# Kernel tuning notes

Measured on AMD Instinct MI355X. Metric: run time of the kernel, lower is better.

## Reference

```python
import jax, jax.numpy as jnp
import numpy as np

N_NODES = 50000


def _sage_conv(x, src, dst, W_l, b_l, W_r, n_nodes):
    # mean-aggregate neighbor (source) features onto targets
    msg = x[src]                                   # [E, d_in] gather
    agg = jax.ops.segment_sum(msg, dst, num_segments=n_nodes)   # [N, d_in]
    deg = jax.ops.segment_sum(jnp.ones((src.shape[0],), x.dtype), dst,
                              num_segments=n_nodes)
    agg = agg / jnp.clip(deg, 1.0, None)[:, None]  # mean with deg>=1 clamp (PyG)
    # out = lin_l(agg) + lin_r(x)   (bias lives in lin_l)
    return agg @ W_l.T + b_l + x @ W_r.T


def setup_inputs() -> dict:
    key = jax.random.key(0)
    ks = jax.random.split(key, 8)
    d_in, d_hid, d_out = 128, 256, 128
    n_edges = 800000
    x = jax.random.normal(ks[0], (N_NODES, d_in), dtype=jnp.float32)
    edge_index = jax.random.randint(ks[1], (2, n_edges), 0, N_NODES, dtype=jnp.int32)
    def glorot(k, shape):
        lim = float(np.sqrt(6.0 / (shape[0] + shape[1])))
        return jax.random.uniform(k, shape, jnp.float32, -lim, lim)
    return {
        "x": x,
        "edge_index": edge_index,
        "W1l": glorot(ks[2], (d_hid, d_in)),
        "b1": jnp.zeros((d_hid,), jnp.float32),
        "W1r": glorot(ks[3], (d_hid, d_in)),
        "W2l": glorot(ks[4], (d_out, d_hid)),
        "b2": jnp.zeros((d_out,), jnp.float32),
        "W2r": glorot(ks[5], (d_out, d_hid)),
    }


def reference(x, edge_index, W1l, b1, W1r, W2l, b2, W2r):
    src, dst = edge_index[0], edge_index[1]
    h = jax.nn.relu(_sage_conv(x, src, dst, W1l, b1, W1r, N_NODES))
    out = _sage_conv(h, src, dst, W2l, b2, W2r, N_NODES)
    return out
```

## Files before the change

kernel.cpp:

```cpp
#include <hip/hip_runtime.h>
#include <hip/hip_bf16.h>

#define NN 50000
#define NN_PAD 50176
#define NE 800000
#define NB 196
#define NB2 784
#define CAP2 1536
#define ECAP 2048
#define EPB 4096

typedef __attribute__((ext_vector_type(8))) short short8;
typedef __attribute__((ext_vector_type(8))) unsigned short ushort8;
typedef __attribute__((ext_vector_type(4))) float f32x4;
typedef __attribute__((ext_vector_type(2))) float f32x2;
typedef __attribute__((ext_vector_type(4))) unsigned int u32x4;
typedef __attribute__((ext_vector_type(2))) unsigned int u32x2;

__device__ __forceinline__ unsigned short f2bf(float f) {
    union { float f; unsigned u; } v; v.f = f;
    unsigned u = v.u;
    return (unsigned short)((u + 0x7fffu + ((u >> 16) & 1u)) >> 16);
}
__device__ __forceinline__ float bfu_lo(unsigned u) {
    union { unsigned u; float f; } v; v.u = u << 16; return v.f;
}
__device__ __forceinline__ float bfu_hi(unsigned u) {
    union { unsigned u; float f; } v; v.u = u & 0xffff0000u; return v.f;
}
__device__ __forceinline__ void acc_fp8(float* acc, uint2 q) {
    f32x2 a0 = __builtin_amdgcn_cvt_pk_f32_fp8(q.x, false);
    f32x2 a1 = __builtin_amdgcn_cvt_pk_f32_fp8(q.x, true);
    f32x2 a2 = __builtin_amdgcn_cvt_pk_f32_fp8(q.y, false);
    f32x2 a3 = __builtin_amdgcn_cvt_pk_f32_fp8(q.y, true);
    acc[0] += a0.x; acc[1] += a0.y; acc[2] += a1.x; acc[3] += a1.y;
    acc[4] += a2.x; acc[5] += a2.y; acc[6] += a3.x; acc[7] += a3.y;
}



__global__ void k_setup_part(const float* __restrict__ W1l, const float* __restrict__ W1r,
                             const float* __restrict__ W2l, const float* __restrict__ W2r,
                             unsigned short* __restrict__ W1pk, unsigned short* __restrict__ W2pk,
                             const float* __restrict__ x, unsigned short* __restrict__ Apk,
                             unsigned char* __restrict__ x_f8,
                             const int* __restrict__ src, const int* __restrict__ dst,
                             int* __restrict__ gcursor, unsigned* __restrict__ pairs) {
    int blk = blockIdx.x, t = threadIdx.x;
    if (blk < NB) {
        __shared__ int cnt[NB2];
        __shared__ int cur[NB2];
        __shared__ int base[NB2];
        for (int k = t; k < NB2; k += 256) { cnt[k] = 0; cur[k] = 0; }
        __syncthreads();
        int e0 = blk * EPB;
        int eend = min(e0 + EPB, NE);
        for (int e = e0 + t; e < eend; e += 256)
            atomicAdd(&cnt[dst[e] >> 6], 1);
        __syncthreads();
        for (int k = t; k < NB2; k += 256)
            if (cnt[k] > 0) base[k] = k * CAP2 + atomicAdd(&gcursor[k], cnt[k]);
        __syncthreads();
        for (int e = e0 + t; e < eend; e += 256) {
            int s = src[e], d = dst[e];
            int bk = d >> 6;
            int pos = base[bk] + atomicAdd(&cur[bk], 1);
            if (pos < (bk + 1) * CAP2) pairs[pos] = ((unsigned)s << 6) | (unsigned)(d & 63);
        }
    } else if (blk < 260) {
        int tid = (blk - 196) * 256 + t;
        int table = tid >> 13;
        int r = tid & 8191;
        int lane = r & 63, ni = (r >> 6) & 3, ks = (r >> 8) & 7, g = r >> 11;
        int lm = lane & 15, lq = lane >> 4;
        int o = g * 64 + ni * 16 + lm;
        int k = ks * 32 + lq * 8;
        unsigned short v[8];
        if (table == 0) {
            if (k < 128) {
#pragma unroll
                for (int j = 0; j < 8; ++j) v[j] = f2bf(W1l[o * 128 + k + j]);
            } else {
#pragma unroll
                for (int j = 0; j < 8; ++j) v[j] = f2bf(W1r[o * 128 + k - 128 + j]);
            }
            *(uint4*)(W1pk + (size_t)r * 8) = *(const uint4*)v;
        } else {
            if (o < 128) {
#pragma unroll
                for (int j = 0; j < 8; ++j) v[j] = f2bf(W2l[o * 256 + k + j]);
            } else {
#pragma unroll
                for (int j = 0; j < 8; ++j) v[j] = f2bf(W2r[(o - 128) * 256 + k + j]);
            }
            *(uint4*)(W2pk + (size_t)r * 8) = *(const uint4*)v;
        }
    } else {
        int gid = (blk - 260) * 256 + t;
        int nq = gid >> 7, r128 = gid & 127;
        int n = nq * 4 + (r128 & 3), c = r128 >> 2;
        f32x4 v = __builtin_nontemporal_load((const f32x4*)x + (size_t)n * 32 + c);
        unsigned short o[4];
        o[0] = f2bf(v[0]); o[1] = f2bf(v[1]); o[2] = f2bf(v[2]); o[3] = f2bf(v[3]);
        int k = 128 + c * 4;
        int ks = k >> 5, lq = (k >> 3) & 3, j0 = k & 7;
        int tile = n >> 6, r = n & 63, mi = r >> 4, lm = r & 15;
        *(u32x2*)(Apk + (size_t)tile * 16384 +
                  ((size_t)((ks * 4 + mi) * 64 + lm + 16 * lq)) * 8 + j0) = *(const u32x2*)o;
        unsigned p = (unsigned)__builtin_amdgcn_cvt_pk_fp8_f32(v[0], v[1], 0, false);
        p = (unsigned)__builtin_amdgcn_cvt_pk_fp8_f32(v[2], v[3], (int)p, true);
        *(unsigned*)(x_f8 + (size_t)n * 128 + c * 4) = p;
    }
}

__global__ __launch_bounds__(512) void k_build_agg1(
        const int* __restrict__ gcursor, const unsigned* __restrict__ pairs,
        const uint2* __restrict__ xf8, unsigned short* __restrict__ esrc,
        unsigned* __restrict__ meta, unsigned short* __restrict__ Apk) {
    __shared__ unsigned lp[CAP2];
    __shared__ __align__(16) unsigned short lsrc[ECAP];
    __shared__ int ldeg[64];
    __shared__ int lcur[64];
    __shared__ int lstart[64];
    int b = blockIdx.x, t = threadIdx.x;
    if (t < 64) ldeg[t] = 0;
    __syncthreads();
    int cnt = min(gcursor[b], CAP2);
    const unsigned* pb = pairs + (size_t)b * CAP2;
    for (int e = t; e < cnt; e += 512) {
        unsigned p = pb[e];
        lp[e] = p;
        atomicAdd(&ldeg[p & 63u], 1);
    }
    __syncthreads();
    if (t < 64) {
        int s = 0;
        for (int j = 0; j < t; ++j) s += (ldeg[j] + 7) & ~7;
        lstart[t] = s; lcur[t] = s;
    }
    __syncthreads();
    for (int e = t; e < cnt; e += 512) {
        unsigned p = lp[e];
        int pos = atomicAdd(&lcur[p & 63u], 1);
        lsrc[pos] = (unsigned short)(p >> 6);
    }
    __syncthreads();
    int lim = lstart[63] + ldeg[63];
    for (int e = t; e < lim; e += 512) esrc[(size_t)b * ECAP + e] = lsrc[e];
    if (t < 64) {
        int node = b * 64 + t;
        if (node < NN)
            meta[node] = ((unsigned)(b * ECAP + lstart[t])) | ((unsigned)ldeg[t] << 21);
    }
    int c = t & 15, h = (t >> 4) & 1;
#pragma unroll
    for (int rr = 0; rr < 4; ++rr) {
        int nl = rr * 16 + (t >> 5);
        int st = lstart[nl], dg = ldeg[nl];
        float acc[8] = {0.f, 0.f, 0.f, 0.f, 0.f, 0.f, 0.f, 0.f};
        int nbt = dg >> 3;
        for (int k = h; k < nbt; k += 2) {
            ushort8 sv = *(const ushort8*)(lsrc + st + k * 8);
            uint2 q0 = xf8[(size_t)sv[0] * 16 + c];
            uint2 q1 = xf8[(size_t)sv[1] * 16 + c];
            uint2 q2 = xf8[(size_t)sv[2] * 16 + c];
            uint2 q3 = xf8[(size_t)sv[3] * 16 + c];
            uint2 q4 = xf8[(size_t)sv[4] * 16 + c];
            uint2 q5 = xf8[(size_t)sv[5] * 16 + c];
            uint2 q6 = xf8[(size_t)sv[6] * 16 + c];
            uint2 q7 = xf8[(size_t)sv[7] * 16 + c];
            acc_fp8(acc, q0); acc_fp8(acc, q1); acc_fp8(acc, q2); acc_fp8(acc, q3);
            acc_fp8(acc, q4); acc_fp8(acc, q5); acc_fp8(acc, q6); acc_fp8(acc, q7);
        }
        if (h == (nbt & 1)) {
            for (int i = nbt * 8; i < dg; ++i)
                acc_fp8(acc, xf8[(size_t)lsrc[st + i] * 16 + c]);
        }
#pragma unroll
        for (int j = 0; j < 8; ++j) acc[j] += __shfl_xor(acc[j], 16);
        if (h == 0) {
            float invd = 1.0f / (float)max(dg, 1);
            unsigned short o[8];
#pragma unroll
            for (int j = 0; j < 8; ++j) o[j] = f2bf(acc[j] * invd);
            int ks = c >> 2, lq = c & 3;
            int mi = nl >> 4, lm = nl & 15;
            *(u32x4*)(Apk + (size_t)b * 16384 +
                      ((size_t)((ks * 4 + mi) * 64 + lm + 16 * lq)) * 8) = *(const u32x4*)o;
        }
    }
}

__global__ __launch_bounds__(256, 2) void k_gemm12(
        const unsigned short* __restrict__ Apk,
        const unsigned short* __restrict__ W1pk, const unsigned short* __restrict__ W2pk,
        const float* __restrict__ b1, const float* __restrict__ b2,
        unsigned char* __restrict__ y2f8, unsigned short* __restrict__ Sbf) {
    __shared__ unsigned short T[16384];
    int t = threadIdx.x, blk = blockIdx.x;
    int wave = t >> 6, lane = t & 63;
    int lm = lane & 15, lq = lane >> 4;
    int pbase = lm * 4 + lq;

    short8 w[8][4];
    {
        const unsigned short* wb = W1pk + (size_t)wave * 16384;
#pragma unroll
        for (int ks = 0; ks < 8; ++ks)
#pragma unroll
            for (int ni = 0; ni < 4; ++ni)
                w[ks][ni] = *(const short8*)(wb + ((size_t)((ks * 4 + ni) * 64 + lane)) * 8);
    }

    const unsigned short* apk = Apk + (size_t)blk * 16384;
    f32x4 acc1[4][4];
#pragma unroll
    for (int mi = 0; mi < 4; ++mi)
#pragma unroll
        for (int ni = 0; ni < 4; ++ni) acc1[mi][ni] = (f32x4){0.f, 0.f, 0.f, 0.f};
#pragma unroll
    for (int ks = 0; ks < 8; ++ks) {
        short8 a[4];
#pragma unroll
        for (int mi = 0; mi < 4; ++mi)
            a[mi] = *(const short8*)(apk + ((size_t)((ks * 4 + mi) * 64 + lane)) * 8);
#pragma unroll
        for (int mi = 0; mi < 4; ++mi)
#pragma unroll
            for (int ni = 0; ni < 4; ++ni)
                acc1[mi][ni] = __builtin_amdgcn_mfma_f32_16x16x32_bf16(a[mi], w[ks][ni], acc1[mi][ni], 0, 0, 0);
    }

    {
        const unsigned short* wb = W2pk + (size_t)wave * 16384;
#pragma unroll
        for (int ks = 0; ks < 8; ++ks)
#pragma unroll
            for (int ni = 0; ni < 4; ++ni)
                w[ks][ni] = *(const short8*)(wb + ((size_t)((ks * 4 + ni) * 64 + lane)) * 8);
    }

#pragma unroll
    for (int ni = 0; ni < 4; ++ni) {
        int col = wave * 64 + ni * 16 + lm;
        float bv = b1[col];
        int ks = col >> 5;
        int la = (col & 31) >> 3, j = col & 7;
#pragma unroll
        for (int mi = 0; mi < 4; ++mi)
#pragma unroll
            for (int r = 0; r < 4; ++r) {
                float v = fmaxf(acc1[mi][ni][r] + bv, 0.0f);
                T[((size_t)((ks * 4 + mi) * 64 + (lq * 4 + r) * 4 + la)) * 8 + j] = f2bf(v);
            }
    }
    __syncthreads();

    f32x4 acc2[4][4];
#pragma unroll
    for (int mi = 0; mi < 4; ++mi)
#pragma unroll
        for (int ni = 0; ni < 4; ++ni) acc2[mi][ni] = (f32x4){0.f, 0.f, 0.f, 0.f};
#pragma unroll
    for (int ks = 0; ks < 8; ++ks) {
        short8 a[4];
#pragma unroll
        for (int mi = 0; mi < 4; ++mi)
            a[mi] = *(const short8*)(T + ((size_t)((ks * 4 + mi) * 64 + pbase)) * 8);
#pragma unroll
        for (int mi = 0; mi < 4; ++mi)
#pragma unroll
            for (int ni = 0; ni < 4; ++ni)
                acc2[mi][ni] = __builtin_amdgcn_mfma_f32_16x16x32_bf16(a[mi], w[ks][ni], acc2[mi][ni], 0, 0, 0);
    }
    __syncthreads();

    {
        unsigned char* T8 = (unsigned char*)T;
        unsigned short* T16 = (unsigned short*)T + 4096;
        if (wave < 2) {
#pragma unroll
            for (int ni = 0; ni < 4; ++ni) {
                int col = wave * 64 + ni * 16 + lm;
#pragma unroll
                for (int mi = 0; mi < 4; ++mi)
#pragma unroll
                    for (int r = 0; r < 4; ++r) {
                        int rl = mi * 16 + lq * 4 + r;
                        float v = acc2[mi][ni][r];
                        unsigned p = (unsigned)__builtin_amdgcn_cvt_pk_fp8_f32(v, v, 0, false);
                        T8[rl * 128 + col] = (unsigned char)(p & 0xff);
                    }
            }
        } else {
#pragma unroll
            for (int ni = 0; ni < 4; ++ni) {
                int col = (wave - 2) * 64 + ni * 16 + lm;
                float bv = b2[col];
#pragma unroll
                for (int mi = 0; mi < 4; ++mi)
#pragma unroll
                    for (int r = 0; r < 4; ++r) {
                        int rl = mi * 16 + lq * 4 + r;
                        T16[rl * 128 + col] = f2bf(acc2[mi][ni][r] + bv);
                    }
            }
        }
    }
    __syncthreads();

    {
        const uint4* Ty = (const uint4*)T;
        uint4* gy = (uint4*)(y2f8 + (size_t)blk * 64 * 128);
        gy[t] = Ty[t];
        gy[t + 256] = Ty[t + 256];
        const u32x4* Ts = (const u32x4*)((const char*)T + 8192);
        u32x4* gs = (u32x4*)(Sbf + (size_t)blk * 64 * 128);
#pragma unroll
        for (int i = 0; i < 4; ++i)
            __builtin_nontemporal_store(Ts[t + i * 256], &gs[t + i * 256]);
    }
}

__global__ void k_agg_out(const uint2* __restrict__ yf8, const unsigned short* __restrict__ Sbf,
                          const unsigned* __restrict__ meta,
                          const unsigned short* __restrict__ esrc,
                          float* __restrict__ out) {
    int gid = blockIdx.x * blockDim.x + threadIdx.x;
    int n = gid >> 5, sub = gid & 31, c = sub & 15, h = sub >> 4;
    unsigned mt = meta[n];
    int st = (int)(mt & 0x1FFFFFu), dg = (int)(mt >> 21);
    float acc[8] = {0.f, 0.f, 0.f, 0.f, 0.f, 0.f, 0.f, 0.f};
    int nbt = dg >> 3;
    for (int k = h; k < nbt; k += 2) {
        ushort8 sv = *(const ushort8*)(esrc + (size_t)st + (size_t)k * 8);
        uint2 q0 = yf8[(size_t)sv[0] * 16 + c];
        uint2 q1 = yf8[(size_t)sv[1] * 16 + c];
        uint2 q2 = yf8[(size_t)sv[2] * 16 + c];
        uint2 q3 = yf8[(size_t)sv[3] * 16 + c];
        uint2 q4 = yf8[(size_t)sv[4] * 16 + c];
        uint2 q5 = yf8[(size_t)sv[5] * 16 + c];
        uint2 q6 = yf8[(size_t)sv[6] * 16 + c];
        uint2 q7 = yf8[(size_t)sv[7] * 16 + c];
        acc_fp8(acc, q0); acc_fp8(acc, q1); acc_fp8(acc, q2); acc_fp8(acc, q3);
        acc_fp8(acc, q4); acc_fp8(acc, q5); acc_fp8(acc, q6); acc_fp8(acc, q7);
    }
    if (h == (nbt & 1)) {
        for (int i = nbt * 8; i < dg; ++i)
            acc_fp8(acc, yf8[(size_t)esrc[st + i] * 16 + c]);
    }
#pragma unroll
    for (int j = 0; j < 8; ++j) acc[j] += __shfl_xor(acc[j], 16);
    float invd = 1.0f / (float)max(dg, 1);
    float s0 = h ? acc[4] : acc[0];
    float s1 = h ? acc[5] : acc[1];
    float s2 = h ? acc[6] : acc[2];
    float s3 = h ? acc[7] : acc[3];
    int colb = c * 8 + h * 4;
    u32x2 sv2 = *(const u32x2*)(Sbf + (size_t)n * 128 + colb);
    f32x4 o;
    o[0] = bfu_lo(sv2[0]) + s0 * invd; o[1] = bfu_hi(sv2[0]) + s1 * invd;
    o[2] = bfu_lo(sv2[1]) + s2 * invd; o[3] = bfu_hi(sv2[1]) + s3 * invd;
    __builtin_nontemporal_store(o, (f32x4*)(out + (size_t)n * 128 + colb));
}

extern "C" void kernel_launch(void* const* d_in, const int* in_sizes, int n_in,
                              void* d_out, int out_size, void* d_ws, size_t ws_size,
                              hipStream_t stream) {
    const float* x   = (const float*)d_in[0];
    const int*   ei  = (const int*)d_in[1];
    const int*   src = ei;
    const int*   dst = ei + NE;
    const float* W1l = (const float*)d_in[2];
    const float* b1  = (const float*)d_in[3];
    const float* W1r = (const float*)d_in[4];
    const float* W2l = (const float*)d_in[5];
    const float* b2  = (const float*)d_in[6];
    const float* W2r = (const float*)d_in[7];
    float* out = (float*)d_out;

    char* ws = (char*)d_ws;
    int* gcursor          = (int*)(ws + 0);
    unsigned* meta        = (unsigned*)(ws + 4096);
    unsigned* pairs       = (unsigned*)(ws + 204800);
    unsigned short* esrc  = (unsigned short*)(ws + 5021696);
    unsigned char* x_f8   = (unsigned char*)(ws + 8232960);
    unsigned short* Sbf   = (unsigned short*)(ws + 14632960);
    unsigned char* y2f8   = (unsigned char*)(ws + 27478016);
    unsigned short* Apk   = (unsigned short*)(ws + 33900544);
    unsigned short* W1pk  = (unsigned short*)(ws + 59590656);
    unsigned short* W2pk  = (unsigned short*)(ws + 59721728);

    hipMemsetAsync(gcursor, 0, 4096, stream);
    k_setup_part<<<6510, 256, 0, stream>>>(W1l, W1r, W2l, W2r, W1pk, W2pk,
                                           x, Apk, x_f8, src, dst, gcursor, pairs);
    k_build_agg1<<<NB2, 512, 0, stream>>>(gcursor, pairs, (const uint2*)x_f8,
                                          esrc, meta, Apk);
    k_gemm12<<<NB2, 256, 0, stream>>>(Apk, W1pk, W2pk, b1, b2, y2f8, Sbf);
    k_agg_out<<<NN * 32 / 256, 256, 0, stream>>>((const uint2*)y2f8, Sbf,
                                                 meta, esrc, out);
}
```

Baseline: 197.1 us.

## Fuse CSR build and layer-1 aggregation into GEMM kernel via LDS A-tile

Merges the per-bucket CSR build and layer-1 mean aggregation into the fused GEMM kernel. The aggregated bf16 rows now go straight into an LDS tile alongside a separately packed self-feature tile, so the aggregated half of the A matrix no longer round-trips through global memory and one launch disappears. Both gather loops drop the two-thread split per feature chunk in favour of one thread per 8-column chunk, which removes the shuffle reduction. The cost is fewer threads covering each node's gather, so each thread walks longer serial loops, and the fused kernel uses 256 threads where the build kernel had 512.

```diff
diff --git a/kernel.cpp b/kernel.cpp
--- a/kernel.cpp
+++ b/kernel.cpp
@@ -42,7 +42,7 @@
 __global__ void k_setup_part(const float* __restrict__ W1l, const float* __restrict__ W1r,
                              const float* __restrict__ W2l, const float* __restrict__ W2r,
                              unsigned short* __restrict__ W1pk, unsigned short* __restrict__ W2pk,
-                             const float* __restrict__ x, unsigned short* __restrict__ Apk,
+                             const float* __restrict__ x, unsigned short* __restrict__ Aslf,
                              unsigned char* __restrict__ x_f8,
                              const int* __restrict__ src, const int* __restrict__ dst,
                              int* __restrict__ gcursor, unsigned* __restrict__ pairs) {
@@ -97,41 +97,41 @@
         }
     } else {
         int gid = (blk - 260) * 256 + t;
-        int nq = gid >> 7, r128 = gid & 127;
-        int n = nq * 4 + (r128 & 3), c = r128 >> 2;
+        int n = gid >> 5, c = gid & 31;
         f32x4 v = __builtin_nontemporal_load((const f32x4*)x + (size_t)n * 32 + c);
         unsigned short o[4];
         o[0] = f2bf(v[0]); o[1] = f2bf(v[1]); o[2] = f2bf(v[2]); o[3] = f2bf(v[3]);
-        int k = 128 + c * 4;
-        int ks = k >> 5, lq = (k >> 3) & 3, j0 = k & 7;
         int tile = n >> 6, r = n & 63, mi = r >> 4, lm = r & 15;
-        *(u32x2*)(Apk + (size_t)tile * 16384 +
-                  ((size_t)((ks * 4 + mi) * 64 + lm + 16 * lq)) * 8 + j0) = *(const u32x2*)o;
+        int ck = (c >> 3) * 4 + mi;
+        int lq = (c >> 1) & 3, j0 = 4 * (c & 1);
+        *(u32x2*)(Aslf + (size_t)tile * 8192 +
+                  ((size_t)(ck * 64 + lm + 16 * lq)) * 8 + j0) = *(const u32x2*)o;
         unsigned p = (unsigned)__builtin_amdgcn_cvt_pk_fp8_f32(v[0], v[1], 0, false);
         p = (unsigned)__builtin_amdgcn_cvt_pk_fp8_f32(v[2], v[3], (int)p, true);
         *(unsigned*)(x_f8 + (size_t)n * 128 + c * 4) = p;
     }
 }
 
-__global__ __launch_bounds__(512) void k_build_agg1(
+__global__ __launch_bounds__(256, 2) void k_bagg_gemm(
         const int* __restrict__ gcursor, const unsigned* __restrict__ pairs,
-        const uint2* __restrict__ xf8, unsigned short* __restrict__ esrc,
-        unsigned* __restrict__ meta, unsigned short* __restrict__ Apk) {
-    __shared__ unsigned lp[CAP2];
+        const uint2* __restrict__ xf8, const unsigned short* __restrict__ Aslf,
+        const unsigned short* __restrict__ W1pk, const unsigned short* __restrict__ W2pk,
+        const float* __restrict__ b1, const float* __restrict__ b2,
+        unsigned short* __restrict__ esrc, unsigned* __restrict__ meta,
+        unsigned char* __restrict__ y2f8, unsigned short* __restrict__ Sbf) {
+    __shared__ unsigned short LA[16384];
     __shared__ __align__(16) unsigned short lsrc[ECAP];
     __shared__ int ldeg[64];
     __shared__ int lcur[64];
     __shared__ int lstart[64];
     int b = blockIdx.x, t = threadIdx.x;
+
     if (t < 64) ldeg[t] = 0;
     __syncthreads();
     int cnt = min(gcursor[b], CAP2);
     const unsigned* pb = pairs + (size_t)b * CAP2;
-    for (int e = t; e < cnt; e += 512) {
-        unsigned p = pb[e];
-        lp[e] = p;
-        atomicAdd(&ldeg[p & 63u], 1);
-    }
+    for (int e = t; e < cnt; e += 256)
+        atomicAdd(&ldeg[pb[e] & 63u], 1);
     __syncthreads();
     if (t < 64) {
         int s = 0;
@@ -139,69 +139,62 @@
         lstart[t] = s; lcur[t] = s;
     }
     __syncthreads();
-    for (int e = t; e < cnt; e += 512) {
-        unsigned p = lp[e];
+    for (int e = t; e < cnt; e += 256) {
+        unsigned p = pb[e];
         int pos = atomicAdd(&lcur[p & 63u], 1);
         lsrc[pos] = (unsigned short)(p >> 6);
     }
     __syncthreads();
     int lim = lstart[63] + ldeg[63];
-    for (int e = t; e < lim; e += 512) esrc[(size_t)b * ECAP + e] = lsrc[e];
+    for (int e = t; e < lim; e += 256) esrc[(size_t)b * ECAP + e] = lsrc[e];
     if (t < 64) {
         int node = b * 64 + t;
         if (node < NN)
             meta[node] = ((unsigned)(b * ECAP + lstart[t])) | ((unsigned)ldeg[t] << 21);
     }
-    int c = t & 15, h = (t >> 4) & 1;
-#pragma unroll
-    for (int rr = 0; rr < 4; ++rr) {
-        int nl = rr * 16 + (t >> 5);
-        int st = lstart[nl], dg = ldeg[nl];
-        float acc[8] = {0.f, 0.f, 0.f, 0.f, 0.f, 0.f, 0.f, 0.f};
-        int nbt = dg >> 3;
-        for (int k = h; k < nbt; k += 2) {
-            ushort8 sv = *(const ushort8*)(lsrc + st + k * 8);
-            uint2 q0 = xf8[(size_t)sv[0] * 16 + c];
-            uint2 q1 = xf8[(size_t)sv[1] * 16 + c];
-            uint2 q2 = xf8[(size_t)sv[2] * 16 + c];
-            uint2 q3 = xf8[(size_t)sv[3] * 16 + c];
-            uint2 q4 = xf8[(size_t)sv[4] * 16 + c];
-            uint2 q5 = xf8[(size_t)sv[5] * 16 + c];
-            uint2 q6 = xf8[(size_t)sv[6] * 16 + c];
-            uint2 q7 = xf8[(size_t)sv[7] * 16 + c];
-            acc_fp8(acc, q0); acc_fp8(acc, q1); acc_fp8(acc, q2); acc_fp8(acc, q3);
-            acc_fp8(acc, q4); acc_fp8(acc, q5); acc_fp8(acc, q6); acc_fp8(acc, q7);
-        }
-        if (h == (nbt & 1)) {
-            for (int i = nbt * 8; i < dg; ++i)
+
+    {
+        int c = t & 15;
+#pragma unroll
+        for (int rr = 0; rr < 4; ++rr) {
+            int nl = rr * 16 + (t >> 4);
+            int st = lstart[nl], dg = ldeg[nl];
+            float acc[8] = {0.f, 0.f, 0.f, 0.f, 0.f, 0.f, 0.f, 0.f};
+            int i = 0;
+            for (; i + 8 <= dg; i += 8) {
+                ushort8 sv = *(const ushort8*)(lsrc + st + i);
+                uint2 q0 = xf8[(size_t)sv[0] * 16 + c];
+                uint2 q1 = xf8[(size_t)sv[1] * 16 + c];
+                uint2 q2 = xf8[(size_t)sv[2] * 16 + c];
+                uint2 q3 = xf8[(size_t)sv[3] * 16 + c];
+                uint2 q4 = xf8[(size_t)sv[4] * 16 + c];
+                uint2 q5 = xf8[(size_t)sv[5] * 16 + c];
+                uint2 q6 = xf8[(size_t)sv[6] * 16 + c];
+                uint2 q7 = xf8[(size_t)sv[7] * 16 + c];
+                acc_fp8(acc, q0); acc_fp8(acc, q1); acc_fp8(acc, q2); acc_fp8(acc, q3);
+                acc_fp8(acc, q4); acc_fp8(acc, q5); acc_fp8(acc, q6); acc_fp8(acc, q7);
+            }
+            for (; i < dg; ++i)
                 acc_fp8(acc, xf8[(size_t)lsrc[st + i] * 16 + c]);
-        }
-#pragma unroll
-        for (int j = 0; j < 8; ++j) acc[j] += __shfl_xor(acc[j], 16);
-        if (h == 0) {
             float invd = 1.0f / (float)max(dg, 1);
             unsigned short o[8];
 #pragma unroll
             for (int j = 0; j < 8; ++j) o[j] = f2bf(acc[j] * invd);
-            int ks = c >> 2, lq = c & 3;
-            int mi = nl >> 4, lm = nl & 15;
-            *(u32x4*)(Apk + (size_t)b * 16384 +
-                      ((size_t)((ks * 4 + mi) * 64 + lm + 16 * lq)) * 8) = *(const u32x4*)o;
+            int ks = c >> 2, lq2 = c & 3;
+            int mi = nl >> 4, lm2 = nl & 15;
+            *(u32x4*)(LA + ((size_t)((ks * 4 + mi) * 64 + lm2 + 16 * lq2)) * 8) = *(const u32x4*)o;
         }
     }
-}
-
-__global__ __launch_bounds__(256, 2) void k_gemm12(
-        const unsigned short* __restrict__ Apk,
-        const unsigned short* __restrict__ W1pk, const unsigned short* __restrict__ W2pk,
-        const float* __restrict__ b1, const float* __restrict__ b2,
-        unsigned char* __restrict__ y2f8, unsigned short* __restrict__ Sbf) {
-    __shared__ unsigned short T[16384];
-    int t = threadIdx.x, blk = blockIdx.x;
+    {
+        const u32x4* g = (const u32x4*)(Aslf + (size_t)b * 8192);
+        u32x4* d = (u32x4*)(LA + 8192);
+#pragma unroll
+        for (int i = 0; i < 4; ++i) d[t + i * 256] = g[t + i * 256];
+    }
+
     int wave = t >> 6, lane = t & 63;
     int lm = lane & 15, lq = lane >> 4;
     int pbase = lm * 4 + lq;
-
     short8 w[8][4];
     {
         const unsigned short* wb = W1pk + (size_t)wave * 16384;
@@ -211,8 +204,8 @@
             for (int ni = 0; ni < 4; ++ni)
                 w[ks][ni] = *(const short8*)(wb + ((size_t)((ks * 4 + ni) * 64 + lane)) * 8);
     }
-
-    const unsigned short* apk = Apk + (size_t)blk * 16384;
+    __syncthreads();
+
     f32x4 acc1[4][4];
 #pragma unroll
     for (int mi = 0; mi < 4; ++mi)
@@ -223,7 +216,7 @@
         short8 a[4];
 #pragma unroll
         for (int mi = 0; mi < 4; ++mi)
-            a[mi] = *(const short8*)(apk + ((size_t)((ks * 4 + mi) * 64 + lane)) * 8);
+            a[mi] = *(const short8*)(LA + ((size_t)((ks * 4 + mi) * 64 + lane)) * 8);
 #pragma unroll
         for (int mi = 0; mi < 4; ++mi)
 #pragma unroll
@@ -239,6 +232,7 @@
             for (int ni = 0; ni < 4; ++ni)
                 w[ks][ni] = *(const short8*)(wb + ((size_t)((ks * 4 + ni) * 64 + lane)) * 8);
     }
+    __syncthreads();
 
 #pragma unroll
     for (int ni = 0; ni < 4; ++ni) {
@@ -251,7 +245,7 @@
 #pragma unroll
             for (int r = 0; r < 4; ++r) {
                 float v = fmaxf(acc1[mi][ni][r] + bv, 0.0f);
-                T[((size_t)((ks * 4 + mi) * 64 + (lq * 4 + r) * 4 + la)) * 8 + j] = f2bf(v);
+                LA[((size_t)((ks * 4 + mi) * 64 + (lq * 4 + r) * 4 + la)) * 8 + j] = f2bf(v);
             }
     }
     __syncthreads();
@@ -266,7 +260,7 @@
         short8 a[4];
 #pragma unroll
         for (int mi = 0; mi < 4; ++mi)
-            a[mi] = *(const short8*)(T + ((size_t)((ks * 4 + mi) * 64 + pbase)) * 8);
+            a[mi] = *(const short8*)(LA + ((size_t)((ks * 4 + mi) * 64 + pbase)) * 8);
 #pragma unroll
         for (int mi = 0; mi < 4; ++mi)
 #pragma unroll
@@ -276,8 +270,8 @@
     __syncthreads();
 
     {
-        unsigned char* T8 = (unsigned char*)T;
-        unsigned short* T16 = (unsigned short*)T + 4096;
+        unsigned char* T8 = (unsigned char*)LA;
+        unsigned short* T16 = (unsigned short*)LA + 4096;
         if (wave < 2) {
 #pragma unroll
             for (int ni = 0; ni < 4; ++ni) {
@@ -310,12 +304,12 @@
     __syncthreads();
 
     {
-        const uint4* Ty = (const uint4*)T;
-        uint4* gy = (uint4*)(y2f8 + (size_t)blk * 64 * 128);
+        const uint4* Ty = (const uint4*)LA;
+        uint4* gy = (uint4*)(y2f8 + (size_t)b * 64 * 128);
         gy[t] = Ty[t];
         gy[t + 256] = Ty[t + 256];
-        const u32x4* Ts = (const u32x4*)((const char*)T + 8192);
-        u32x4* gs = (u32x4*)(Sbf + (size_t)blk * 64 * 128);
+        const u32x4* Ts = (const u32x4*)((const char*)LA + 8192);
+        u32x4* gs = (u32x4*)(Sbf + (size_t)b * 64 * 128);
 #pragma unroll
         for (int i = 0; i < 4; ++i)
             __builtin_nontemporal_store(Ts[t + i * 256], &gs[t + i * 256]);
@@ -327,13 +321,13 @@
                           const unsigned short* __restrict__ esrc,
                           float* __restrict__ out) {
     int gid = blockIdx.x * blockDim.x + threadIdx.x;
-    int n = gid >> 5, sub = gid & 31, c = sub & 15, h = sub >> 4;
+    int n = gid >> 4, c = gid & 15;
     unsigned mt = meta[n];
     int st = (int)(mt & 0x1FFFFFu), dg = (int)(mt >> 21);
     float acc[8] = {0.f, 0.f, 0.f, 0.f, 0.f, 0.f, 0.f, 0.f};
-    int nbt = dg >> 3;
-    for (int k = h; k < nbt; k += 2) {
-        ushort8 sv = *(const ushort8*)(esrc + (size_t)st + (size_t)k * 8);
+    int i = 0;
+    for (; i + 8 <= dg; i += 8) {
+        ushort8 sv = *(const ushort8*)(esrc + (size_t)st + i);
         uint2 q0 = yf8[(size_t)sv[0] * 16 + c];
         uint2 q1 = yf8[(size_t)sv[1] * 16 + c];
         uint2 q2 = yf8[(size_t)sv[2] * 16 + c];
@@ -345,23 +339,20 @@
         acc_fp8(acc, q0); acc_fp8(acc, q1); acc_fp8(acc, q2); acc_fp8(acc, q3);
         acc_fp8(acc, q4); acc_fp8(acc, q5); acc_fp8(acc, q6); acc_fp8(acc, q7);
     }
-    if (h == (nbt & 1)) {
-        for (int i = nbt * 8; i < dg; ++i)
-            acc_fp8(acc, yf8[(size_t)esrc[st + i] * 16 + c]);
-    }
-#pragma unroll
-    for (int j = 0; j < 8; ++j) acc[j] += __shfl_xor(acc[j], 16);
+    for (; i < dg; ++i) {
+        int s = esrc[st + i];
+        acc_fp8(acc, yf8[(size_t)s * 16 + c]);
+    }
     float invd = 1.0f / (float)max(dg, 1);
-    float s0 = h ? acc[4] : acc[0];
-    float s1 = h ? acc[5] : acc[1];
-    float s2 = h ? acc[6] : acc[2];
-    float s3 = h ? acc[7] : acc[3];
-    int colb = c * 8 + h * 4;
-    u32x2 sv2 = *(const u32x2*)(Sbf + (size_t)n * 128 + colb);
-    f32x4 o;
-    o[0] = bfu_lo(sv2[0]) + s0 * invd; o[1] = bfu_hi(sv2[0]) + s1 * invd;
-    o[2] = bfu_lo(sv2[1]) + s2 * invd; o[3] = bfu_hi(sv2[1]) + s3 * invd;
-    __builtin_nontemporal_store(o, (f32x4*)(out + (size_t)n * 128 + colb));
+    u32x4 sv = __builtin_nontemporal_load((const u32x4*)Sbf + (size_t)n * 16 + c);
+    f32x4 o0, o1;
+    o0[0] = bfu_lo(sv[0]) + acc[0] * invd; o0[1] = bfu_hi(sv[0]) + acc[1] * invd;
+    o0[2] = bfu_lo(sv[1]) + acc[2] * invd; o0[3] = bfu_hi(sv[1]) + acc[3] * invd;
+    o1[0] = bfu_lo(sv[2]) + acc[4] * invd; o1[1] = bfu_hi(sv[2]) + acc[5] * invd;
+    o1[2] = bfu_lo(sv[3]) + acc[6] * invd; o1[3] = bfu_hi(sv[3]) + acc[7] * invd;
+    f32x4* op = (f32x4*)(out + (size_t)n * 128 + c * 8);
+    __builtin_nontemporal_store(o0, op);
+    __builtin_nontemporal_store(o1, op + 1);
 }
 
 extern "C" void kernel_launch(void* const* d_in, const int* in_sizes, int n_in,
@@ -387,16 +378,15 @@
     unsigned char* x_f8   = (unsigned char*)(ws + 8232960);
     unsigned short* Sbf   = (unsigned short*)(ws + 14632960);
     unsigned char* y2f8   = (unsigned char*)(ws + 27478016);
-    unsigned short* Apk   = (unsigned short*)(ws + 33900544);
-    unsigned short* W1pk  = (unsigned short*)(ws + 59590656);
-    unsigned short* W2pk  = (unsigned short*)(ws + 59721728);
+    unsigned short* Aslf  = (unsigned short*)(ws + 33900544);
+    unsigned short* W1pk  = (unsigned short*)(ws + 46745600);
+    unsigned short* W2pk  = (unsigned short*)(ws + 46876672);
 
     hipMemsetAsync(gcursor, 0, 4096, stream);
     k_setup_part<<<6510, 256, 0, stream>>>(W1l, W1r, W2l, W2r, W1pk, W2pk,
-                                           x, Apk, x_f8, src, dst, gcursor, pairs);
-    k_build_agg1<<<NB2, 512, 0, stream>>>(gcursor, pairs, (const uint2*)x_f8,
-                                          esrc, meta, Apk);
-    k_gemm12<<<NB2, 256, 0, stream>>>(Apk, W1pk, W2pk, b1, b2, y2f8, Sbf);
-    k_agg_out<<<NN * 32 / 256, 256, 0, stream>>>((const uint2*)y2f8, Sbf,
+                                           x, Aslf, x_f8, src, dst, gcursor, pairs);
+    k_bagg_gemm<<<NB2, 256, 0, stream>>>(gcursor, pairs, (const uint2*)x_f8, Aslf,
+                                         W1pk, W2pk, b1, b2, esrc, meta, y2f8, Sbf);
+    k_agg_out<<<NN * 16 / 256, 256, 0, stream>>>((const uint2*)y2f8, Sbf,
                                                  meta, esrc, out);
 }
```

Measured after the change: 191.7 us. 2.7% less time.
